# Performance work log

Hardware: AMD Instinct MI355X
Metric: run time of the kernel (lower is better)

## Reference

```python
import jax, jax.numpy as jnp
import numpy as np

S, B, H = 2048, 2, 1024
NH = 16
HD = H // NH
EPS = 1e-5


def _ln(z, w, b):
    m = jnp.mean(z, axis=-1, keepdims=True)
    v = jnp.mean(jnp.square(z - m), axis=-1, keepdims=True)
    return (z - m) * jax.lax.rsqrt(v + EPS) * w + b


def setup_inputs() -> dict:
    key = jax.random.key(0)
    ks = jax.random.split(key, 8)
    std = 0.02
    return {
        "x": jax.random.normal(ks[0], (S, B, H), dtype=jnp.float32),
        "ln1_w": jnp.ones((H,), jnp.float32),
        "ln1_b": jnp.zeros((H,), jnp.float32),
        "w_qkv": jax.random.normal(ks[1], (3 * H, H), jnp.float32) * std,
        "b_qkv": jnp.zeros((3 * H,), jnp.float32),
        "w_proj": jax.random.normal(ks[2], (H, H), jnp.float32) * std,
        "b_proj": jnp.zeros((H,), jnp.float32),
        "ln2_w": jnp.ones((H,), jnp.float32),
        "ln2_b": jnp.zeros((H,), jnp.float32),
        "w_fc1": jax.random.normal(ks[3], (4 * H, H), jnp.float32) * std,
        "b_fc1": jnp.zeros((4 * H,), jnp.float32),
        "w_fc2": jax.random.normal(ks[4], (H, 4 * H), jnp.float32) * std,
        "b_fc2": jnp.zeros((H,), jnp.float32),
    }


def reference(x, ln1_w, ln1_b, w_qkv, b_qkv, w_proj, b_proj,
              ln2_w, ln2_b, w_fc1, b_fc1, w_fc2, b_fc2):
    s, b, h = x.shape
    # --- LayerNormLinear: LN then fused QKV projection ---
    residual = x
    qkv = _ln(x, ln1_w, ln1_b) @ w_qkv.T + b_qkv            # [S, B, 3H]
    # per-head interleaved packing: [S, B, NH, 3*HD] then split on last dim
    qkv = qkv.reshape(s, b, NH, 3 * HD).transpose(1, 2, 0, 3)  # [B, NH, S, 3HD]
    q, k, v = jnp.split(qkv, 3, axis=3)                      # each [B, NH, S, HD]
    # --- naive causal attention with full SxS scores ---
    scores = jnp.einsum("bhsd,bhtd->bhst", q, k) * (HD ** -0.5)
    causal = jnp.triu(jnp.ones((s, s), dtype=bool), k=1)
    scores = jnp.where(causal, -jnp.inf, scores)
    attn = jax.nn.softmax(scores, axis=-1)                   # [B, NH, S, S]
    out = jnp.einsum("bhst,bhtd->bhsd", attn, v)             # [B, NH, S, HD]
    out = out.transpose(0, 2, 1, 3).reshape(b, s, h).transpose(1, 0, 2)  # [S, B, H]
    out = out @ w_proj.T + b_proj
    x = residual + out
    # --- LayerNormMLP: LN -> fc1 -> gelu(tanh) -> fc2, residual ---
    residual = x
    hmid = jax.nn.gelu(_ln(x, ln2_w, ln2_b) @ w_fc1.T + b_fc1, approximate=True)
    x = residual + (hmid @ w_fc2.T + b_fc2)
    return x
```

## Files before the change

kernel.cpp:

```cpp
#include <hip/hip_runtime.h>
#include <math.h>

#define S_LEN 2048
#define B_SZ 2
#define NHEAD 16
#define HDIM 64
#define H_DIM 1024
#define M_ROWS (S_LEN * B_SZ)
#define LN_EPS 1e-5f
#define KSTR 72
#define SCL 0.18033688011112042f

typedef __attribute__((ext_vector_type(4))) float f32x4;
typedef __attribute__((ext_vector_type(8))) short short8;
typedef __attribute__((ext_vector_type(8))) unsigned short u16x8;
typedef __attribute__((ext_vector_type(4))) unsigned short u16x4;
typedef __attribute__((ext_vector_type(2))) unsigned short u16x2;

__device__ __forceinline__ float bf2f(unsigned short u) {
    return __uint_as_float(((unsigned int)u) << 16);
}
__device__ __forceinline__ unsigned short f2bf(float f) {
    unsigned int u = __float_as_uint(f);
    return (unsigned short)((u + 0x7fffu + ((u >> 16) & 1u)) >> 16);
}
__device__ __forceinline__ void gld_lds16(const void* g, void* l) {
    __builtin_amdgcn_global_load_lds(
        (const __attribute__((address_space(1))) void*)g,
        (__attribute__((address_space(3))) void*)l, 16, 0, 0);
}

__global__ __launch_bounds__(256) void cast_all(const float* __restrict__ wqkv,
                                                const float* __restrict__ wproj,
                                                const float* __restrict__ wfc1,
                                                const float* __restrict__ wfc2,
                                                unsigned short* __restrict__ oqkv,
                                                unsigned short* __restrict__ oproj,
                                                unsigned short* __restrict__ ofc1,
                                                unsigned short* __restrict__ ofc2) {
    const int i = blockIdx.x * 256 + threadIdx.x;
    const float* src; unsigned short* dst; int off;
    if (i < 786432)       { src = wqkv;  dst = oqkv;  off = i; }
    else if (i < 1048576) { src = wproj; dst = oproj; off = i - 786432; }
    else if (i < 2097152) { src = wfc1;  dst = ofc1;  off = i - 1048576; }
    else                  { src = wfc2;  dst = ofc2;  off = i - 2097152; }
    f32x4 v = ((const f32x4*)src)[off];
    u16x4 o;
    o.x = f2bf(v.x); o.y = f2bf(v.y); o.z = f2bf(v.z); o.w = f2bf(v.w);
    ((u16x4*)dst)[off] = o;
}

__global__ __launch_bounds__(256) void ln_bf16(const float* __restrict__ x,
                                               const float* __restrict__ w,
                                               const float* __restrict__ b,
                                               unsigned short* __restrict__ y) {
    const int m = blockIdx.x;
    const int tid = threadIdx.x;
    const float* row = x + (size_t)m * H_DIM;

    float4 v = ((const float4*)row)[tid];
    float s  = v.x + v.y + v.z + v.w;
    float ss = v.x * v.x + v.y * v.y + v.z * v.z + v.w * v.w;

    __shared__ float rs[4], rss[4], stats[2];
    const int wave = tid >> 6, lane = tid & 63;
    for (int off = 32; off; off >>= 1) {
        s  += __shfl_down(s, off);
        ss += __shfl_down(ss, off);
    }
    if (lane == 0) { rs[wave] = s; rss[wave] = ss; }
    __syncthreads();
    if (tid == 0) {
        float S = rs[0] + rs[1] + rs[2] + rs[3];
        float SS = rss[0] + rss[1] + rss[2] + rss[3];
        float mean = S * (1.0f / H_DIM);
        float var = SS * (1.0f / H_DIM) - mean * mean;
        stats[0] = mean;
        stats[1] = rsqrtf(var + LN_EPS);
    }
    __syncthreads();
    const float mean = stats[0], inv = stats[1];
    float4 wv = ((const float4*)w)[tid];
    float4 bv = ((const float4*)b)[tid];
    u16x4 o;
    o.x = f2bf((v.x - mean) * inv * wv.x + bv.x);
    o.y = f2bf((v.y - mean) * inv * wv.y + bv.y);
    o.z = f2bf((v.z - mean) * inv * wv.z + bv.z);
    o.w = f2bf((v.w - mean) * inv * wv.w + bv.w);
    ((u16x4*)(y + (size_t)m * H_DIM))[tid] = o;
}

template <int EPI, bool BF_OUT, int TN>
__global__ __launch_bounds__(256) void gemm_mfma(const unsigned short* __restrict__ A,
                                                 const unsigned short* __restrict__ B,
                                                 const float* __restrict__ bias,
                                                 const float* __restrict__ resid,
                                                 void* __restrict__ Cout,
                                                 int M, int N, int K) {
    constexpr int NJ = TN / 32;
    __shared__ __attribute__((aligned(16))) unsigned short As[2][128 * 32];
    __shared__ __attribute__((aligned(16))) unsigned short Bs[2][TN * 32];

    const int tid = threadIdx.x;
    const int wid = tid >> 6;
    const int ln  = tid & 63;
    const int quad = ln >> 4;
    const int mr   = ln & 15;
    const int wm = (wid >> 1) * 64;
    const int wn = (wid & 1) * (TN / 2);

    const int mb = M >> 7;
    const int stripe = mb >> 3;
    const int xcd = blockIdx.x & 7;
    const int local = blockIdx.x >> 3;
    const int m0 = (xcd * stripe + (local % stripe)) << 7;
    const int n0 = (local / stripe) * TN;

    const int c  = wid * 64 + ln;
    const int r0 = c >> 2;
    const int k0 = (c & 3) * 8;
    const unsigned short* gA0 = A + (size_t)(m0 + r0) * K + k0;
    const unsigned short* gA1 = A + (size_t)(m0 + 64 + r0) * K + k0;
    const unsigned short* gB0 = B + (size_t)(n0 + r0) * K + k0;
    const unsigned short* gB1 = B + (size_t)(n0 + 64 + r0) * K + k0;
    const int lo0 = wid * 512;
    const int lo1 = 2048 + wid * 512;

    const f32x4 zero = {0.f, 0.f, 0.f, 0.f};
    f32x4 acc[4][NJ];
#pragma unroll
    for (int i = 0; i < 4; i++)
#pragma unroll
        for (int j = 0; j < NJ; j++) acc[i][j] = zero;

    const int nt = K >> 5;
    gld_lds16(gA0, As[0] + lo0);
    gld_lds16(gA1, As[0] + lo1);
    gld_lds16(gB0, Bs[0] + lo0);
    if constexpr (TN == 128) gld_lds16(gB1, Bs[0] + lo1);

    for (int kt = 0; kt < nt; kt++) {
        __syncthreads();
        const int nxt = kt + 1;
        if (nxt < nt) {
            const int nb_ = nxt & 1;
            const int koff = nxt * 32;
            gld_lds16(gA0 + koff, As[nb_] + lo0);
            gld_lds16(gA1 + koff, As[nb_] + lo1);
            gld_lds16(gB0 + koff, Bs[nb_] + lo0);
            if constexpr (TN == 128) gld_lds16(gB1 + koff, Bs[nb_] + lo1);
        }
        const unsigned short* as = As[kt & 1];
        const unsigned short* bs = Bs[kt & 1];
        short8 af[4], bfr[NJ];
#pragma unroll
        for (int i = 0; i < 4; i++)
            af[i] = *(const short8*)(as + (wm + i * 16 + mr) * 32 + quad * 8);
#pragma unroll
        for (int j = 0; j < NJ; j++)
            bfr[j] = *(const short8*)(bs + (wn + j * 16 + mr) * 32 + quad * 8);
#pragma unroll
        for (int i = 0; i < 4; i++)
#pragma unroll
            for (int j = 0; j < NJ; j++)
                acc[i][j] = __builtin_amdgcn_mfma_f32_16x16x32_bf16(bfr[j], af[i], acc[i][j], 0, 0, 0);
    }

    f32x4 bias4[NJ];
#pragma unroll
    for (int j = 0; j < NJ; j++)
        bias4[j] = *(const f32x4*)(bias + n0 + wn + j * 16 + quad * 4);

#pragma unroll
    for (int i = 0; i < 4; i++) {
        const int m = m0 + wm + i * 16 + mr;
#pragma unroll
        for (int j = 0; j < NJ; j++) {
            const int nb = n0 + wn + j * 16 + quad * 4;
            f32x4 v = acc[i][j] + bias4[j];
            if (EPI == 1) v += *(const f32x4*)(resid + (size_t)m * N + nb);
            if (EPI == 2) {
#pragma unroll
                for (int r = 0; r < 4; r++) {
                    const float t = v[r];
                    v[r] = 0.5f * t * (1.0f + tanhf(0.7978845608f * (t + 0.044715f * t * t * t)));
                }
            }
            if (BF_OUT) {
                u16x4 pk;
                pk.x = f2bf(v.x); pk.y = f2bf(v.y); pk.z = f2bf(v.z); pk.w = f2bf(v.w);
                *(u16x4*)((unsigned short*)Cout + (size_t)m * N + nb) = pk;
            } else {
                *(f32x4*)((float*)Cout + (size_t)m * N + nb) = v;
            }
        }
    }
}

__global__ __launch_bounds__(256) void attn_mfma(const unsigned short* __restrict__ qkv,
                                                 unsigned short* __restrict__ out) {
    __shared__ __attribute__((aligned(16))) unsigned short Ks[64 * KSTR];
    __shared__ __attribute__((aligned(16))) unsigned short Vs[64 * KSTR];
    __shared__ __attribute__((aligned(16))) unsigned short Ps[64 * KSTR];

    const int tid = threadIdx.x;
    const int wid = tid >> 6;
    const int ln  = tid & 63;
    const int quad = ln >> 4;
    const int mr   = ln & 15;

    const int id = blockIdx.x;
    const int local = id >> 3;
    const int bh = (id & 7) * 4 + (local >> 4);
    const int pa = local & 15;
    const int b  = bh >> 4;
    const int nh = bh & 15;
    const size_t chan = (size_t)nh * 192;

    const int ksr = tid >> 2, ksc = tid & 3;
    const int vt0 = (tid & 31) * 2, vd0 = (tid >> 5) * 8;

    u16x8 kp0, kp1, vp0, vp1;

#pragma unroll
    for (int half = 0; half < 2; half++) {
        const int qt = half ? (31 - pa) : pa;
        const int qb = qt * 64;

        short8 qf0, qf1;
        {
            const int qrow = qb + wid * 16 + mr;
            const unsigned short* gq = qkv + ((size_t)(qrow * 2 + b)) * 3072 + chan + quad * 8;
            qf0 = *(const short8*)gq;
            qf1 = *(const short8*)(gq + 32);
        }

        const f32x4 zero = {0.f, 0.f, 0.f, 0.f};
        f32x4 o[4];
        float ps = 0.f;
#pragma unroll
        for (int d = 0; d < 4; d++) o[d] = zero;

        {
            const unsigned short* gk = qkv + ((size_t)(ksr * 2 + b)) * 3072 + chan + 64 + ksc * 16;
            kp0 = *(const u16x8*)gk;
            kp1 = *(const u16x8*)(gk + 8);
            const unsigned short* gv = qkv + ((size_t)(vt0 * 2 + b)) * 3072 + chan + 128 + vd0;
            vp0 = *(const u16x8*)gv;
            vp1 = *(const u16x8*)(gv + 6144);
        }

        for (int kt = 0; kt <= qt; kt++) {
            __syncthreads();
            *(u16x8*)(Ks + ksr * KSTR + ksc * 16) = kp0;
            *(u16x8*)(Ks + ksr * KSTR + ksc * 16 + 8) = kp1;
#pragma unroll
            for (int j = 0; j < 8; j++) {
                u16x2 pr; pr.x = vp0[j]; pr.y = vp1[j];
                *(u16x2*)(Vs + (vd0 + j) * KSTR + vt0) = pr;
            }
            if (kt < qt) {
                const int nb = (kt + 1) * 64;
                const unsigned short* gk =
                    qkv + ((size_t)((nb + ksr) * 2 + b)) * 3072 + chan + 64 + ksc * 16;
                kp0 = *(const u16x8*)gk;
                kp1 = *(const u16x8*)(gk + 8);
                const unsigned short* gv =
                    qkv + ((size_t)((nb + vt0) * 2 + b)) * 3072 + chan + 128 + vd0;
                vp0 = *(const u16x8*)gv;
                vp1 = *(const u16x8*)(gv + 6144);
            }
            __syncthreads();

            f32x4 sacc[4];
#pragma unroll
            for (int n = 0; n < 4; n++) {
                sacc[n] = zero;
                const unsigned short* kb = Ks + (n * 16 + mr) * KSTR + quad * 8;
                short8 kfr0 = *(const short8*)kb;
                short8 kfr1 = *(const short8*)(kb + 32);
                sacc[n] = __builtin_amdgcn_mfma_f32_16x16x32_bf16(kfr0, qf0, sacc[n], 0, 0, 0);
                sacc[n] = __builtin_amdgcn_mfma_f32_16x16x32_bf16(kfr1, qf1, sacc[n], 0, 0, 0);
            }
            if (kt == qt) {
#pragma unroll
                for (int n = 0; n < 4; n++)
#pragma unroll
                    for (int r = 0; r < 4; r++)
                        if (n * 16 + quad * 4 + r > wid * 16 + mr) sacc[n][r] = -3.0e38f;
            }

            unsigned short* prow = Ps + (wid * 16 + mr) * KSTR + quad * 4;
#pragma unroll
            for (int n = 0; n < 4; n++) {
                u16x4 pk;
#pragma unroll
                for (int r = 0; r < 4; r++) {
                    const float p = exp2f(fminf(sacc[n][r] * SCL, 80.f));
                    ps += p;
                    pk[r] = (unsigned short)(__float_as_uint(p) >> 16);
                }
                *(u16x4*)(prow + n * 16) = pk;
            }

            {
                const unsigned short* pb = Ps + (wid * 16 + mr) * KSTR + quad * 8;
                short8 pa0 = *(const short8*)pb;
                short8 pa1 = *(const short8*)(pb + 32);
#pragma unroll
                for (int d = 0; d < 4; d++) {
                    const unsigned short* vb = Vs + (d * 16 + mr) * KSTR + quad * 8;
                    short8 vf0 = *(const short8*)vb;
                    short8 vf1 = *(const short8*)(vb + 32);
                    o[d] = __builtin_amdgcn_mfma_f32_16x16x32_bf16(vf0, pa0, o[d], 0, 0, 0);
                    o[d] = __builtin_amdgcn_mfma_f32_16x16x32_bf16(vf1, pa1, o[d], 0, 0, 0);
                }
            }
        }

        ps += __shfl_xor(ps, 16);
        ps += __shfl_xor(ps, 32);
        const float inv = 1.0f / ps;
        const int qrow = qb + wid * 16 + mr;
        unsigned short* po = out + ((size_t)(qrow * 2 + b)) * H_DIM + nh * HDIM;
#pragma unroll
        for (int d = 0; d < 4; d++) {
            u16x4 pk;
#pragma unroll
            for (int r = 0; r < 4; r++) pk[r] = f2bf(o[d][r] * inv);
            *(u16x4*)(po + d * 16 + quad * 4) = pk;
        }
    }
}

extern "C" void kernel_launch(void* const* d_in, const int* in_sizes, int n_in,
                              void* d_out, int out_size, void* d_ws, size_t ws_size,
                              hipStream_t stream) {
    const float* x      = (const float*)d_in[0];
    const float* ln1_w  = (const float*)d_in[1];
    const float* ln1_b  = (const float*)d_in[2];
    const float* w_qkv  = (const float*)d_in[3];
    const float* b_qkv  = (const float*)d_in[4];
    const float* w_proj = (const float*)d_in[5];
    const float* b_proj = (const float*)d_in[6];
    const float* ln2_w  = (const float*)d_in[7];
    const float* ln2_b  = (const float*)d_in[8];
    const float* w_fc1  = (const float*)d_in[9];
    const float* b_fc1  = (const float*)d_in[10];
    const float* w_fc2  = (const float*)d_in[11];
    const float* b_fc2  = (const float*)d_in[12];
    float* out = (float*)d_out;

    char* ws = (char*)d_ws;
    unsigned short* wqkv_bf  = (unsigned short*)(ws);
    unsigned short* wproj_bf = (unsigned short*)(ws + ((size_t)6 << 20));
    unsigned short* wfc1_bf  = (unsigned short*)(ws + ((size_t)8 << 20));
    unsigned short* wfc2_bf  = (unsigned short*)(ws + ((size_t)16 << 20));
    unsigned short* ln_buf   = (unsigned short*)(ws + ((size_t)24 << 20));
    unsigned short* qkv_bf   = (unsigned short*)(ws + ((size_t)32 << 20));
    unsigned short* attn_bf  = (unsigned short*)(ws + ((size_t)56 << 20));
    unsigned short* fc1_bf   = (unsigned short*)(ws + ((size_t)32 << 20));

    cast_all<<<12288, 256, 0, stream>>>(w_qkv, w_proj, w_fc1, w_fc2,
                                        wqkv_bf, wproj_bf, wfc1_bf, wfc2_bf);

    ln_bf16<<<M_ROWS, 256, 0, stream>>>(x, ln1_w, ln1_b, ln_buf);
    gemm_mfma<0, true, 128><<<768, 256, 0, stream>>>(
        ln_buf, wqkv_bf, b_qkv, nullptr, qkv_bf, M_ROWS, 3072, 1024);
    attn_mfma<<<512, 256, 0, stream>>>(qkv_bf, attn_bf);
    gemm_mfma<1, false, 64><<<512, 256, 0, stream>>>(
        attn_bf, wproj_bf, b_proj, x, out, M_ROWS, 1024, 1024);
    ln_bf16<<<M_ROWS, 256, 0, stream>>>(out, ln2_w, ln2_b, ln_buf);
    gemm_mfma<2, true, 128><<<1024, 256, 0, stream>>>(
        ln_buf, wfc1_bf, b_fc1, nullptr, fc1_bf, M_ROWS, 4096, 1024);
    gemm_mfma<1, false, 64><<<512, 256, 0, stream>>>(
        fc1_bf, wfc2_bf, b_fc2, out, out, M_ROWS, 1024, 4096);
}
```

Baseline: 375.0 us.

## Stage GEMM tiles through registers with padded LDS and BK=64

Replaces the double-buffered direct global-to-LDS loads in the MFMA GEMM with register prefetch of the next tile, stored into a single padded LDS buffer. The K tile grows from 32 to 64 and the LDS row stride is padded to 72 to avoid bank conflicts on fragment reads. The aim is fewer barriers per unit of K and conflict-free LDS reads. In exchange it uses more registers and adds two barriers per iteration around the single-buffer store.

```diff
diff --git a/kernel.cpp b/kernel.cpp
--- a/kernel.cpp
+++ b/kernel.cpp
@@ -23,11 +23,6 @@
 __device__ __forceinline__ unsigned short f2bf(float f) {
     unsigned int u = __float_as_uint(f);
     return (unsigned short)((u + 0x7fffu + ((u >> 16) & 1u)) >> 16);
-}
-__device__ __forceinline__ void gld_lds16(const void* g, void* l) {
-    __builtin_amdgcn_global_load_lds(
-        (const __attribute__((address_space(1))) void*)g,
-        (__attribute__((address_space(3))) void*)l, 16, 0, 0);
 }
 
 __global__ __launch_bounds__(256) void cast_all(const float* __restrict__ wqkv,
@@ -98,8 +93,10 @@
                                                  void* __restrict__ Cout,
                                                  int M, int N, int K) {
     constexpr int NJ = TN / 32;
-    __shared__ __attribute__((aligned(16))) unsigned short As[2][128 * 32];
-    __shared__ __attribute__((aligned(16))) unsigned short Bs[2][TN * 32];
+    constexpr int ST = 72;
+    constexpr int BNR = (TN == 128) ? 4 : 2;
+    __shared__ __attribute__((aligned(16))) unsigned short As[128 * ST];
+    __shared__ __attribute__((aligned(16))) unsigned short Bs[TN * ST];
 
     const int tid = threadIdx.x;
     const int wid = tid >> 6;
@@ -116,15 +113,29 @@
     const int m0 = (xcd * stripe + (local % stripe)) << 7;
     const int n0 = (local / stripe) * TN;
 
-    const int c  = wid * 64 + ln;
-    const int r0 = c >> 2;
-    const int k0 = (c & 3) * 8;
-    const unsigned short* gA0 = A + (size_t)(m0 + r0) * K + k0;
-    const unsigned short* gA1 = A + (size_t)(m0 + 64 + r0) * K + k0;
-    const unsigned short* gB0 = B + (size_t)(n0 + r0) * K + k0;
-    const unsigned short* gB1 = B + (size_t)(n0 + 64 + r0) * K + k0;
-    const int lo0 = wid * 512;
-    const int lo1 = 2048 + wid * 512;
+    const int ar = tid >> 1, aks = (tid & 1) * 32;
+    const unsigned short* gA = A + (size_t)(m0 + ar) * K + aks;
+    unsigned short* lA = As + ar * ST + aks;
+    const int br  = (TN == 128) ? (tid >> 1) : (tid >> 2);
+    const int bks = (TN == 128) ? ((tid & 1) * 32) : ((tid & 3) * 16);
+    const unsigned short* gB = B + (size_t)(n0 + br) * K + bks;
+    unsigned short* lB = Bs + br * ST + bks;
+
+    u16x8 apf[4], bpf[BNR];
+    auto load_tile = [&](int kt) {
+        const unsigned short* pa = gA + kt * 64;
+#pragma unroll
+        for (int r = 0; r < 4; r++) apf[r] = *(const u16x8*)(pa + r * 8);
+        const unsigned short* pb = gB + kt * 64;
+#pragma unroll
+        for (int r = 0; r < BNR; r++) bpf[r] = *(const u16x8*)(pb + r * 8);
+    };
+    auto store_tile = [&]() {
+#pragma unroll
+        for (int r = 0; r < 4; r++) *(u16x8*)(lA + r * 8) = apf[r];
+#pragma unroll
+        for (int r = 0; r < BNR; r++) *(u16x8*)(lB + r * 8) = bpf[r];
+    };
 
     const f32x4 zero = {0.f, 0.f, 0.f, 0.f};
     f32x4 acc[4][NJ];
@@ -133,37 +144,34 @@
 #pragma unroll
         for (int j = 0; j < NJ; j++) acc[i][j] = zero;
 
-    const int nt = K >> 5;
-    gld_lds16(gA0, As[0] + lo0);
-    gld_lds16(gA1, As[0] + lo1);
-    gld_lds16(gB0, Bs[0] + lo0);
-    if constexpr (TN == 128) gld_lds16(gB1, Bs[0] + lo1);
+    const int nt = K >> 6;
+    load_tile(0);
+    store_tile();
+    if (nt > 1) load_tile(1);
+    __syncthreads();
 
     for (int kt = 0; kt < nt; kt++) {
-        __syncthreads();
-        const int nxt = kt + 1;
-        if (nxt < nt) {
-            const int nb_ = nxt & 1;
-            const int koff = nxt * 32;
-            gld_lds16(gA0 + koff, As[nb_] + lo0);
-            gld_lds16(gA1 + koff, As[nb_] + lo1);
-            gld_lds16(gB0 + koff, Bs[nb_] + lo0);
-            if constexpr (TN == 128) gld_lds16(gB1 + koff, Bs[nb_] + lo1);
-        }
-        const unsigned short* as = As[kt & 1];
-        const unsigned short* bs = Bs[kt & 1];
-        short8 af[4], bfr[NJ];
-#pragma unroll
-        for (int i = 0; i < 4; i++)
-            af[i] = *(const short8*)(as + (wm + i * 16 + mr) * 32 + quad * 8);
-#pragma unroll
-        for (int j = 0; j < NJ; j++)
-            bfr[j] = *(const short8*)(bs + (wn + j * 16 + mr) * 32 + quad * 8);
-#pragma unroll
-        for (int i = 0; i < 4; i++)
+#pragma unroll
+        for (int h = 0; h < 2; h++) {
+            short8 af[4], bf[NJ];
+#pragma unroll
+            for (int i = 0; i < 4; i++)
+                af[i] = *(const short8*)(As + (wm + i * 16 + mr) * ST + h * 32 + quad * 8);
 #pragma unroll
             for (int j = 0; j < NJ; j++)
-                acc[i][j] = __builtin_amdgcn_mfma_f32_16x16x32_bf16(bfr[j], af[i], acc[i][j], 0, 0, 0);
+                bf[j] = *(const short8*)(Bs + (wn + j * 16 + mr) * ST + h * 32 + quad * 8);
+#pragma unroll
+            for (int i = 0; i < 4; i++)
+#pragma unroll
+                for (int j = 0; j < NJ; j++)
+                    acc[i][j] = __builtin_amdgcn_mfma_f32_16x16x32_bf16(bf[j], af[i], acc[i][j], 0, 0, 0);
+        }
+        if (kt + 1 < nt) {
+            __syncthreads();
+            store_tile();
+            if (kt + 2 < nt) load_tile(kt + 2);
+            __syncthreads();
+        }
     }
 
     f32x4 bias4[NJ];
```

Result: faster. 356.9 us (-4.8%).
